# Kernel optimization log

Measured on AMD Instinct MI355X. Metric: run time of the kernel, lower is better.

Reference implementation:

```python
import jax, jax.numpy as jnp
import numpy as np

N, K, NC, D = 32768, 4096, 4, 256


def setup_inputs() -> dict:
    key = jax.random.key(0)
    k1, k2, k3 = jax.random.split(key, 3)
    x = jax.random.normal(k1, (N, D), dtype=jnp.float32)
    mu = jax.random.normal(k2, (K, NC, D), dtype=jnp.float32)
    # std must be positive (it is inverted); uniform in [0.5, 1.5)
    std = jax.random.uniform(k3, (D,), dtype=jnp.float32) + 0.5
    return {"x": x, "mu": mu, "std": std}


def reference(x, mu, std):
    # Gaussian density eval: exp(-0.5 * sum_d (x_nd - mu_k0d)^2 / std_d)
    # Expanded algebraically to avoid the (N, K, D) intermediate:
    #   ||x - mu||^2_w = x^2 . w + mu^2 . w - 2 * x . (mu * w),  w = 1/std
    inv_std = 1.0 / std                       # (D,)
    mu0 = mu[:, 0, :]                          # (K, D) -- only component 0 is used
    x_sq = jnp.einsum("nd,d->n", x * x, inv_std)          # (N,)
    mu_sq = jnp.einsum("kd,d->k", mu0 * mu0, inv_std)     # (K,)
    cross = jnp.einsum("nd,kd->nk", x, mu0 * inv_std)     # (N, K) GEMM
    logits = -0.5 * (x_sq[:, None] + mu_sq[None, :] - 2.0 * cross)
    return jnp.exp(logits)                                 # (N, K)
```

## Files before the change

### kernel.cpp

```cpp
#include <hip/hip_runtime.h>

#define N_ 32768
#define K_ 4096
#define NC_ 4
#define D_ 256

using floatx4 = __attribute__((ext_vector_type(4))) float;
using bf16x8  = __attribute__((ext_vector_type(8))) short;

__device__ __forceinline__ unsigned short f2bf(float f) {
  union { float f; unsigned u; } a;
  a.f = f;
  unsigned u = a.u;
  u += 0x7fffu + ((u >> 16) & 1u);
  return (unsigned short)(u >> 16);
}

__device__ __forceinline__ void async_copy16(void* lds, const void* g) {
  __builtin_amdgcn_global_load_lds(
      (__attribute__((address_space(1))) void*)(g),
      (__attribute__((address_space(3))) void*)(lds),
      16, 0, 0);
}

template <bool WRITE_BF>
__global__ void prep_x_kern(const float* __restrict__ x, const float* __restrict__ sd,
                            unsigned short* __restrict__ xb, float* __restrict__ xsq) {
  const int lane = threadIdx.x & 63;
  const int row  = blockIdx.x * 4 + (threadIdx.x >> 6);
  const float4 xv = reinterpret_cast<const float4*>(x + (size_t)row * D_)[lane];
  const float4 sv = reinterpret_cast<const float4*>(sd)[lane];
  const float i0 = 1.0f / sv.x, i1 = 1.0f / sv.y, i2 = 1.0f / sv.z, i3 = 1.0f / sv.w;
  float s = xv.x * xv.x * i0 + xv.y * xv.y * i1 + xv.z * xv.z * i2 + xv.w * xv.w * i3;
  if (WRITE_BF) {
    union { unsigned short u[4]; uint2 v; } p;
    p.u[0] = f2bf(xv.x); p.u[1] = f2bf(xv.y); p.u[2] = f2bf(xv.z); p.u[3] = f2bf(xv.w);
    reinterpret_cast<uint2*>(xb)[(size_t)row * 64 + lane] = p.v;
  }
#pragma unroll
  for (int off = 32; off > 0; off >>= 1) s += __shfl_down(s, off, 64);
  if (lane == 0) xsq[row] = s;
}

template <bool WRITE_BF>
__global__ void prep_mu_kern(const float* __restrict__ mu, const float* __restrict__ sd,
                             unsigned short* __restrict__ bb, float* __restrict__ musq) {
  const int lane = threadIdx.x & 63;
  const int row  = blockIdx.x * 4 + (threadIdx.x >> 6);
  const float4 mv = reinterpret_cast<const float4*>(mu + (size_t)row * (NC_ * D_))[lane];
  const float4 sv = reinterpret_cast<const float4*>(sd)[lane];
  const float i0 = 1.0f / sv.x, i1 = 1.0f / sv.y, i2 = 1.0f / sv.z, i3 = 1.0f / sv.w;
  float s = mv.x * mv.x * i0 + mv.y * mv.y * i1 + mv.z * mv.z * i2 + mv.w * mv.w * i3;
  if (WRITE_BF) {
    union { unsigned short u[4]; uint2 v; } p;
    p.u[0] = f2bf(mv.x * i0); p.u[1] = f2bf(mv.y * i1);
    p.u[2] = f2bf(mv.z * i2); p.u[3] = f2bf(mv.w * i3);
    reinterpret_cast<uint2*>(bb)[(size_t)row * 64 + lane] = p.v;
  }
#pragma unroll
  for (int off = 32; off > 0; off >>= 1) s += __shfl_down(s, off, 64);
  if (lane == 0) musq[row] = s;
}

__global__ void gauss_mfma(const unsigned short* __restrict__ xb,
                           const unsigned short* __restrict__ bb,
                           const float* __restrict__ xsq,
                           const float* __restrict__ musq,
                           float* __restrict__ out) {
  constexpr int BM = 128, BN = 128, BK = 32;
  __shared__ __align__(16) unsigned short As[BM * BK];
  __shared__ __align__(16) unsigned short Bs[BN * BK];
  const int tid  = threadIdx.x;
  const int wave = tid >> 6, lane = tid & 63;
  const int wm = wave >> 1, wn = wave & 1;
  const int rowBase = blockIdx.y * BM;
  const int colBase = blockIdx.x * BN;

  const int srow = lane >> 2;
  const int scol = (lane & 3) * 8;
  const unsigned short* gA0 = xb + (size_t)(rowBase + wave * 16 + srow) * D_ + scol;
  const unsigned short* gA1 = gA0 + (size_t)64 * D_;
  const unsigned short* gB0 = bb + (size_t)(colBase + wave * 16 + srow) * D_ + scol;
  const unsigned short* gB1 = gB0 + (size_t)64 * D_;
  unsigned short* lA0 = &As[(wave * 16) * BK];
  unsigned short* lA1 = &As[(wave * 16 + 64) * BK];
  unsigned short* lB0 = &Bs[(wave * 16) * BK];
  unsigned short* lB1 = &Bs[(wave * 16 + 64) * BK];

  floatx4 acc[4][4] = {};
  const int fr = lane & 15;
  const int fk = (lane >> 4) * 8;

#pragma unroll
  for (int kt = 0; kt < D_ / BK; ++kt) {
    __syncthreads();
    async_copy16(lA0, gA0 + kt * BK);
    async_copy16(lA1, gA1 + kt * BK);
    async_copy16(lB0, gB0 + kt * BK);
    async_copy16(lB1, gB1 + kt * BK);
    __syncthreads();
    bf16x8 af[4], bfv[4];
#pragma unroll
    for (int i = 0; i < 4; ++i)
      af[i] = *reinterpret_cast<const bf16x8*>(&As[(wm * 64 + i * 16 + fr) * BK + fk]);
#pragma unroll
    for (int j = 0; j < 4; ++j)
      bfv[j] = *reinterpret_cast<const bf16x8*>(&Bs[(wn * 64 + j * 16 + fr) * BK + fk]);
#pragma unroll
    for (int i = 0; i < 4; ++i)
#pragma unroll
      for (int j = 0; j < 4; ++j)
        acc[i][j] = __builtin_amdgcn_mfma_f32_16x16x32_bf16(af[i], bfv[j], acc[i][j], 0, 0, 0);
  }

  const int q = lane >> 4, c = lane & 15;
  float ms[4];
#pragma unroll
  for (int j = 0; j < 4; ++j) ms[j] = musq[colBase + wn * 64 + j * 16 + c];
#pragma unroll
  for (int i = 0; i < 4; ++i) {
#pragma unroll
    for (int r = 0; r < 4; ++r) {
      const int row = rowBase + wm * 64 + i * 16 + q * 4 + r;
      const float xs = xsq[row];
      float* orow = out + (size_t)row * K_ + colBase + wn * 64 + c;
#pragma unroll
      for (int j = 0; j < 4; ++j)
        orow[j * 16] = __expf(acc[i][j][r] - 0.5f * (xs + ms[j]));
    }
  }
}

__global__ void gauss_mfma_fused(const float* __restrict__ x, const float* __restrict__ mu,
                                 const float* __restrict__ sd,
                                 const float* __restrict__ xsq, const float* __restrict__ musq,
                                 float* __restrict__ out) {
  constexpr int BM = 128, BN = 128, BK = 32;
  __shared__ __align__(16) unsigned short As[BM * BK];
  __shared__ __align__(16) unsigned short Bs[BN * BK];
  __shared__ float invs[D_];
  const int tid = threadIdx.x;
  invs[tid] = 1.0f / sd[tid];
  const int wave = tid >> 6, lane = tid & 63;
  const int wm = wave >> 1, wn = wave & 1;
  const int rowBase = blockIdx.y * BM;
  const int colBase = blockIdx.x * BN;
  const int srow = tid >> 1;
  const int scol = (tid & 1) * 16;
  const float* gA = x + (size_t)(rowBase + srow) * D_ + scol;
  const float* gB = mu + (size_t)(colBase + srow) * (NC_ * D_) + scol;
  __syncthreads();

  floatx4 acc[4][4] = {};
  const int fr = lane & 15;
  const int fk = (lane >> 4) * 8;

  for (int kt = 0; kt < D_ / BK; ++kt) {
    const int k0 = kt * BK;
    float4 a0 = *(const float4*)(gA + k0);
    float4 a1 = *(const float4*)(gA + k0 + 4);
    float4 a2 = *(const float4*)(gA + k0 + 8);
    float4 a3 = *(const float4*)(gA + k0 + 12);
    float4 b0 = *(const float4*)(gB + k0);
    float4 b1 = *(const float4*)(gB + k0 + 4);
    float4 b2 = *(const float4*)(gB + k0 + 8);
    float4 b3 = *(const float4*)(gB + k0 + 12);
    float fa[16] = {a0.x, a0.y, a0.z, a0.w, a1.x, a1.y, a1.z, a1.w,
                    a2.x, a2.y, a2.z, a2.w, a3.x, a3.y, a3.z, a3.w};
    float fb[16] = {b0.x, b0.y, b0.z, b0.w, b1.x, b1.y, b1.z, b1.w,
                    b2.x, b2.y, b2.z, b2.w, b3.x, b3.y, b3.z, b3.w};
    union { unsigned short u[8]; uint4 v; } pa0, pa1, pb0, pb1;
#pragma unroll
    for (int t = 0; t < 8; ++t) {
      pa0.u[t] = f2bf(fa[t]);
      pa1.u[t] = f2bf(fa[t + 8]);
      pb0.u[t] = f2bf(fb[t] * invs[k0 + scol + t]);
      pb1.u[t] = f2bf(fb[t + 8] * invs[k0 + scol + t + 8]);
    }
    __syncthreads();
    *(uint4*)&As[srow * BK + scol]     = pa0.v;
    *(uint4*)&As[srow * BK + scol + 8] = pa1.v;
    *(uint4*)&Bs[srow * BK + scol]     = pb0.v;
    *(uint4*)&Bs[srow * BK + scol + 8] = pb1.v;
    __syncthreads();
    bf16x8 af[4], bfv[4];
#pragma unroll
    for (int i = 0; i < 4; ++i)
      af[i] = *reinterpret_cast<const bf16x8*>(&As[(wm * 64 + i * 16 + fr) * BK + fk]);
#pragma unroll
    for (int j = 0; j < 4; ++j)
      bfv[j] = *reinterpret_cast<const bf16x8*>(&Bs[(wn * 64 + j * 16 + fr) * BK + fk]);
#pragma unroll
    for (int i = 0; i < 4; ++i)
#pragma unroll
      for (int j = 0; j < 4; ++j)
        acc[i][j] = __builtin_amdgcn_mfma_f32_16x16x32_bf16(af[i], bfv[j], acc[i][j], 0, 0, 0);
  }

  const int q = lane >> 4, c = lane & 15;
  float ms[4];
#pragma unroll
  for (int j = 0; j < 4; ++j) ms[j] = musq[colBase + wn * 64 + j * 16 + c];
#pragma unroll
  for (int i = 0; i < 4; ++i) {
#pragma unroll
    for (int r = 0; r < 4; ++r) {
      const int row = rowBase + wm * 64 + i * 16 + q * 4 + r;
      const float xs = xsq[row];
      float* orow = out + (size_t)row * K_ + colBase + wn * 64 + c;
#pragma unroll
      for (int j = 0; j < 4; ++j)
        orow[j * 16] = __expf(acc[i][j][r] - 0.5f * (xs + ms[j]));
    }
  }
}

__global__ void gauss_naive(const float* __restrict__ x, const float* __restrict__ mu,
                            const float* __restrict__ sd, float* __restrict__ out) {
  const int k = blockIdx.x * 256 + threadIdx.x;
  const int n = blockIdx.y;
  const float* xr = x + (size_t)n * D_;
  const float* mr = mu + (size_t)k * (NC_ * D_);
  float s = 0.0f;
  for (int d = 0; d < D_; ++d) {
    const float diff = xr[d] - mr[d];
    s += diff * diff / sd[d];
  }
  out[(size_t)n * K_ + k] = __expf(-0.5f * s);
}

extern "C" void kernel_launch(void* const* d_in, const int* in_sizes, int n_in,
                              void* d_out, int out_size, void* d_ws, size_t ws_size,
                              hipStream_t stream) {
  const float* x  = (const float*)d_in[0];
  const float* mu = (const float*)d_in[1];
  const float* sd = (const float*)d_in[2];
  float* out = (float*)d_out;

  const size_t xb_bytes   = (size_t)N_ * D_ * 2;
  const size_t bb_bytes   = (size_t)K_ * D_ * 2;
  const size_t xsq_bytes  = (size_t)N_ * 4;
  const size_t musq_bytes = (size_t)K_ * 4;

  dim3 grid_gemm(K_ / 128, N_ / 128);
  if (ws_size >= xb_bytes + bb_bytes + xsq_bytes + musq_bytes) {
    unsigned short* xb = (unsigned short*)d_ws;
    unsigned short* bb = (unsigned short*)((char*)d_ws + xb_bytes);
    float* xsq  = (float*)((char*)d_ws + xb_bytes + bb_bytes);
    float* musq = (float*)((char*)d_ws + xb_bytes + bb_bytes + xsq_bytes);
    prep_x_kern<true><<<N_ / 4, 256, 0, stream>>>(x, sd, xb, xsq);
    prep_mu_kern<true><<<K_ / 4, 256, 0, stream>>>(mu, sd, bb, musq);
    gauss_mfma<<<grid_gemm, 256, 0, stream>>>(xb, bb, xsq, musq, out);
  } else if (ws_size >= xsq_bytes + musq_bytes) {
    float* xsq  = (float*)d_ws;
    float* musq = (float*)((char*)d_ws + xsq_bytes);
    prep_x_kern<false><<<N_ / 4, 256, 0, stream>>>(x, sd, nullptr, xsq);
    prep_mu_kern<false><<<K_ / 4, 256, 0, stream>>>(mu, sd, nullptr, musq);
    gauss_mfma_fused<<<grid_gemm, 256, 0, stream>>>(x, mu, sd, xsq, musq, out);
  } else {
    gauss_naive<<<dim3(K_ / 256, N_), 256, 0, stream>>>(x, mu, sd, out);
  }
}
```

Before: 626.0 us.

## Replace LDS-tiled GEMM with register-direct per-wave tiles and nontemporal stores

The shared-memory staged 128x128 block GEMM is replaced by a kernel where each wave independently computes a 64x64 tile. It loads bf16 fragments straight from global memory into registers with double buffering, so there are no LDS copies and no block barriers. The output is written with nontemporal stores to avoid polluting the cache with the large (N,K) result, and launch bounds request 3 blocks per SM. The cost is less operand reuse per block (each wave reloads its own A and B), which relies on L2/L1 caching. The block-to-tile mapping groups 4 waves along rows sharing one column tile.

```diff
diff --git a/kernel.cpp b/kernel.cpp
--- a/kernel.cpp
+++ b/kernel.cpp
@@ -14,13 +14,6 @@
   unsigned u = a.u;
   u += 0x7fffu + ((u >> 16) & 1u);
   return (unsigned short)(u >> 16);
-}
-
-__device__ __forceinline__ void async_copy16(void* lds, const void* g) {
-  __builtin_amdgcn_global_load_lds(
-      (__attribute__((address_space(1))) void*)(g),
-      (__attribute__((address_space(3))) void*)(lds),
-      16, 0, 0);
 }
 
 template <bool WRITE_BF>
@@ -62,71 +55,63 @@
   if (lane == 0) musq[row] = s;
 }
 
-__global__ void gauss_mfma(const unsigned short* __restrict__ xb,
-                           const unsigned short* __restrict__ bb,
-                           const float* __restrict__ xsq,
-                           const float* __restrict__ musq,
-                           float* __restrict__ out) {
-  constexpr int BM = 128, BN = 128, BK = 32;
-  __shared__ __align__(16) unsigned short As[BM * BK];
-  __shared__ __align__(16) unsigned short Bs[BN * BK];
-  const int tid  = threadIdx.x;
-  const int wave = tid >> 6, lane = tid & 63;
-  const int wm = wave >> 1, wn = wave & 1;
-  const int rowBase = blockIdx.y * BM;
-  const int colBase = blockIdx.x * BN;
-
-  const int srow = lane >> 2;
-  const int scol = (lane & 3) * 8;
-  const unsigned short* gA0 = xb + (size_t)(rowBase + wave * 16 + srow) * D_ + scol;
-  const unsigned short* gA1 = gA0 + (size_t)64 * D_;
-  const unsigned short* gB0 = bb + (size_t)(colBase + wave * 16 + srow) * D_ + scol;
-  const unsigned short* gB1 = gB0 + (size_t)64 * D_;
-  unsigned short* lA0 = &As[(wave * 16) * BK];
-  unsigned short* lA1 = &As[(wave * 16 + 64) * BK];
-  unsigned short* lB0 = &Bs[(wave * 16) * BK];
-  unsigned short* lB1 = &Bs[(wave * 16 + 64) * BK];
-
-  floatx4 acc[4][4] = {};
+__global__ __launch_bounds__(256, 3) void gauss_reg(
+    const unsigned short* __restrict__ xb, const unsigned short* __restrict__ bb,
+    const float* __restrict__ xsq, const float* __restrict__ musq,
+    float* __restrict__ out) {
+  const int wave = threadIdx.x >> 6, lane = threadIdx.x & 63;
+  const int b = blockIdx.x;
+  const int colT = b >> 7;
+  const int rowT = ((b & 127) << 2) | wave;
+  const int row0 = rowT * 64;
+  const int col0 = colT * 64;
+
   const int fr = lane & 15;
   const int fk = (lane >> 4) * 8;
-
-#pragma unroll
-  for (int kt = 0; kt < D_ / BK; ++kt) {
-    __syncthreads();
-    async_copy16(lA0, gA0 + kt * BK);
-    async_copy16(lA1, gA1 + kt * BK);
-    async_copy16(lB0, gB0 + kt * BK);
-    async_copy16(lB1, gB1 + kt * BK);
-    __syncthreads();
-    bf16x8 af[4], bfv[4];
+  const unsigned short* pA = xb + (size_t)(row0 + fr) * D_ + fk;
+  const unsigned short* pB = bb + (size_t)(col0 + fr) * D_ + fk;
+
+  floatx4 acc[4][4] = {};
+  bf16x8 af[2][4], bfv[2][4];
+#pragma unroll
+  for (int i = 0; i < 4; ++i) {
+    af[0][i]  = *reinterpret_cast<const bf16x8*>(pA + (size_t)(i * 16) * D_);
+    bfv[0][i] = *reinterpret_cast<const bf16x8*>(pB + (size_t)(i * 16) * D_);
+  }
+#pragma unroll
+  for (int kt = 0; kt < D_ / 32; ++kt) {
+    const int cur = kt & 1, nxt = cur ^ 1;
+    if (kt < D_ / 32 - 1) {
+      const int ko = (kt + 1) * 32;
+#pragma unroll
+      for (int i = 0; i < 4; ++i) {
+        af[nxt][i]  = *reinterpret_cast<const bf16x8*>(pA + (size_t)(i * 16) * D_ + ko);
+        bfv[nxt][i] = *reinterpret_cast<const bf16x8*>(pB + (size_t)(i * 16) * D_ + ko);
+      }
+    }
 #pragma unroll
     for (int i = 0; i < 4; ++i)
-      af[i] = *reinterpret_cast<const bf16x8*>(&As[(wm * 64 + i * 16 + fr) * BK + fk]);
-#pragma unroll
-    for (int j = 0; j < 4; ++j)
-      bfv[j] = *reinterpret_cast<const bf16x8*>(&Bs[(wn * 64 + j * 16 + fr) * BK + fk]);
-#pragma unroll
-    for (int i = 0; i < 4; ++i)
-#pragma unroll
-      for (int j = 0; j < 4; ++j)
-        acc[i][j] = __builtin_amdgcn_mfma_f32_16x16x32_bf16(af[i], bfv[j], acc[i][j], 0, 0, 0);
+#pragma unroll
+      for (int j = 0; j < 4; ++j)
+        acc[i][j] = __builtin_amdgcn_mfma_f32_16x16x32_bf16(af[cur][i], bfv[cur][j],
+                                                            acc[i][j], 0, 0, 0);
   }
 
   const int q = lane >> 4, c = lane & 15;
   float ms[4];
 #pragma unroll
-  for (int j = 0; j < 4; ++j) ms[j] = musq[colBase + wn * 64 + j * 16 + c];
+  for (int j = 0; j < 4; ++j) ms[j] = musq[col0 + j * 16 + c];
 #pragma unroll
   for (int i = 0; i < 4; ++i) {
 #pragma unroll
     for (int r = 0; r < 4; ++r) {
-      const int row = rowBase + wm * 64 + i * 16 + q * 4 + r;
+      const int row = row0 + i * 16 + q * 4 + r;
       const float xs = xsq[row];
-      float* orow = out + (size_t)row * K_ + colBase + wn * 64 + c;
-#pragma unroll
-      for (int j = 0; j < 4; ++j)
-        orow[j * 16] = __expf(acc[i][j][r] - 0.5f * (xs + ms[j]));
+      float* orow = out + (size_t)row * K_ + col0 + c;
+#pragma unroll
+      for (int j = 0; j < 4; ++j)
+        __builtin_nontemporal_store(__expf(acc[i][j][r] - 0.5f * (xs + ms[j])),
+                                    orow + j * 16);
     }
   }
 }
@@ -242,7 +227,6 @@
   const size_t xsq_bytes  = (size_t)N_ * 4;
   const size_t musq_bytes = (size_t)K_ * 4;
 
-  dim3 grid_gemm(K_ / 128, N_ / 128);
   if (ws_size >= xb_bytes + bb_bytes + xsq_bytes + musq_bytes) {
     unsigned short* xb = (unsigned short*)d_ws;
     unsigned short* bb = (unsigned short*)((char*)d_ws + xb_bytes);
@@ -250,13 +234,13 @@
     float* musq = (float*)((char*)d_ws + xb_bytes + bb_bytes + xsq_bytes);
     prep_x_kern<true><<<N_ / 4, 256, 0, stream>>>(x, sd, xb, xsq);
     prep_mu_kern<true><<<K_ / 4, 256, 0, stream>>>(mu, sd, bb, musq);
-    gauss_mfma<<<grid_gemm, 256, 0, stream>>>(xb, bb, xsq, musq, out);
+    gauss_reg<<<(N_ / 64) * (K_ / 64) / 4, 256, 0, stream>>>(xb, bb, xsq, musq, out);
   } else if (ws_size >= xsq_bytes + musq_bytes) {
     float* xsq  = (float*)d_ws;
     float* musq = (float*)((char*)d_ws + xsq_bytes);
     prep_x_kern<false><<<N_ / 4, 256, 0, stream>>>(x, sd, nullptr, xsq);
     prep_mu_kern<false><<<K_ / 4, 256, 0, stream>>>(mu, sd, nullptr, musq);
-    gauss_mfma_fused<<<grid_gemm, 256, 0, stream>>>(x, mu, sd, xsq, musq, out);
+    gauss_mfma_fused<<<dim3(K_ / 128, N_ / 128), 256, 0, stream>>>(x, mu, sd, xsq, musq, out);
   } else {
     gauss_naive<<<dim3(K_ / 256, N_), 256, 0, stream>>>(x, mu, sd, out);
   }
```

Result: slower. 735.7 us (+17.5%).
